# Optimization experiments

Measured on AMD Instinct MI355X. Metric: run time of the kernel, lower is better.

## Reference

```python
import jax, jax.numpy as jnp
import numpy as np

N = 50000      # nodes
E = 800000     # edges (avg degree 16)
IN = 128       # in_channels
OUT = 128      # out_channels


def setup_inputs() -> dict:
    key = jax.random.key(0)
    k1, k2, k3 = jax.random.split(key, 3)
    x = jax.random.normal(k1, (N, IN), dtype=jnp.float32)
    edge_index = jax.random.randint(k2, (2, E), 0, N, dtype=jnp.int32)
    # GCNConv params: glorot-ish linear weight + zero bias
    W = jax.random.normal(k3, (IN, OUT), dtype=jnp.float32) / np.float32(np.sqrt(IN))
    b = jnp.zeros((OUT,), dtype=jnp.float32)
    return {"x": x, "W": W, "b": b, "edge_index": edge_index}


def reference(x, W, b, edge_index):
    n = x.shape[0]
    src, dst = edge_index[0], edge_index[1]
    # add self loops (GCNConv default add_self_loops=True)
    loop = jnp.arange(n, dtype=edge_index.dtype)
    src = jnp.concatenate([src, loop])
    dst = jnp.concatenate([dst, loop])
    # symmetric normalization: deg^{-1/2}[src] * deg^{-1/2}[dst], deg from dst (flow source_to_target)
    deg = jax.ops.segment_sum(jnp.ones_like(dst, dtype=x.dtype), dst, num_segments=n)
    dinv = jnp.where(deg > 0, jax.lax.rsqrt(jnp.maximum(deg, 1.0)), 0.0)
    norm = dinv[src] * dinv[dst]                     # [E+N]
    xw = x @ W                                       # [N, OUT] dense GEMM first (as GCNConv does)
    msg = xw[src] * norm[:, None]                    # [E+N, OUT] gather + scale
    out = jax.ops.segment_sum(msg, dst, num_segments=n)  # scatter-add aggregate
    return out + b
```

## Files before the change

kernel.cpp:

```cpp
#include <hip/hip_runtime.h>


constexpr int CH = 128;
constexpr int CHUNK = 4096;
constexpr int NCMAX = 256;
constexpr int HP = 256;

typedef __attribute__((ext_vector_type(8))) short short8;
typedef __attribute__((ext_vector_type(4))) float f32x4;

static __device__ __forceinline__ ushort f2bf(float f) {
    unsigned u = __float_as_uint(f);
    u += 0x7fff + ((u >> 16) & 1);
    return (ushort)(u >> 16);
}


__global__ __launch_bounds__(256) void hist_packw(const int* __restrict__ dst,
        int* __restrict__ h, int* __restrict__ coltot,
        const float* __restrict__ Wm, ushort* __restrict__ Wp,
        int E, int nc, int nblk) {
    int t = threadIdx.x, b = blockIdx.x;
    if (b >= nblk) {
        int tid = (b - nblk) * 256 + t;
        if (tid < 2048) {
            int col = tid >> 4, ch16 = tid & 15;
            ushort tmp[8];
            #pragma unroll
            for (int i = 0; i < 8; ++i)
                tmp[i] = f2bf(Wm[(size_t)(ch16 * 8 + i) * CH + col]);
            int d = col * 16 + (ch16 ^ (col & 7));
            *(uint4*)&Wp[(size_t)d * 8] = *(uint4*)tmp;
        }
        return;
    }
    __shared__ int hh[NCMAX];
    for (int i = t; i < NCMAX; i += 256) hh[i] = 0;
    __syncthreads();
    int s = b * CHUNK, e = min(E, s + CHUNK);
    for (int i = s + t * 4; i < e; i += 1024) {
        if (i + 4 <= e) {
            int4 v = *(const int4*)&dst[i];
            atomicAdd(&hh[v.x >> 8], 1);
            atomicAdd(&hh[v.y >> 8], 1);
            atomicAdd(&hh[v.z >> 8], 1);
            atomicAdd(&hh[v.w >> 8], 1);
        } else {
            for (int k = i; k < e; ++k) atomicAdd(&hh[dst[k] >> 8], 1);
        }
    }
    __syncthreads();
    for (int i = t; i < nc; i += 256) {
        int v = hh[i];
        h[(size_t)i * HP + b] = v;
        if (v) atomicAdd(&coltot[i], v);
    }
}


__global__ __launch_bounds__(256) void binscatter_gemm(const int* __restrict__ src,
        const int* __restrict__ dst, const int* __restrict__ h,
        const int* __restrict__ coltot, unsigned* __restrict__ ebuf,
        const float* __restrict__ x, const ushort* __restrict__ Wp,
        ushort* __restrict__ xwd, int E, int N, int nc, int nblk) {
    __shared__ alignas(16) ushort Wlds[16384];
    int t = threadIdx.x, b = blockIdx.x;

    if (b < nblk) {
        int* smc = (int*)Wlds;
        int* cur = smc + 256;
        smc[t] = (t < nc) ? coltot[t] : 0;
        __syncthreads();
        #pragma unroll
        for (int d = 1; d < 256; d <<= 1) {
            int u = (t >= d) ? smc[t - d] : 0;
            __syncthreads();
            smc[t] += u;
            __syncthreads();
        }
        if (t < nc) {
            int base = (t > 0) ? smc[t - 1] : 0;
            const int* hp = &h[(size_t)t * HP];
            int pfx = 0;
            int j = 0;
            for (; j + 4 <= b; j += 4) {
                int4 v = *(const int4*)&hp[j];
                pfx += v.x + v.y + v.z + v.w;
            }
            for (; j < b; ++j) pfx += hp[j];
            cur[t] = base + pfx;
        }
        __syncthreads();
        int s = b * CHUNK, e = min(E, s + CHUNK);
        for (int i = s + t; i < e; i += 256) {
            int d = dst[i];
            int pos = atomicAdd(&cur[d >> 8], 1);
            ebuf[pos] = (unsigned)src[i] | ((unsigned)(d & 255) << 16);
        }
        return;
    }

    int gb = b - nblk;
    int wv = t >> 6, l = t & 63;
    int c15 = l & 15, kc = l >> 4;
    int row0 = gb * 64 + wv * 16;
    int r = row0 + c15;
    bool valid = r < N;

    short8 af[4];
    #pragma unroll
    for (int ks = 0; ks < 4; ++ks) {
        float4 a0 = make_float4(0.f,0.f,0.f,0.f), a1 = a0;
        if (valid) {
            const float* p = x + (size_t)r * CH + ks * 32 + kc * 8;
            a0 = *(const float4*)p;
            a1 = *(const float4*)(p + 4);
        }
        short8 v;
        v[0]=f2bf(a0.x); v[1]=f2bf(a0.y); v[2]=f2bf(a0.z); v[3]=f2bf(a0.w);
        v[4]=f2bf(a1.x); v[5]=f2bf(a1.y); v[6]=f2bf(a1.z); v[7]=f2bf(a1.w);
        af[ks] = v;
    }

    #pragma unroll
    for (int i = 0; i < 8; ++i) {
        int idx = i * 256 + t;
        *(uint4*)&Wlds[idx * 8] = *(const uint4*)&Wp[idx * 8];
    }
    __syncthreads();

    f32x4 acc[8];
    #pragma unroll
    for (int ct = 0; ct < 8; ++ct) { f32x4 z = {0.f,0.f,0.f,0.f}; acc[ct] = z; }

    int swz = l & 7;
    #pragma unroll
    for (int ks = 0; ks < 4; ++ks) {
        #pragma unroll
        for (int ct = 0; ct < 8; ++ct) {
            int col = ct * 16 + c15;
            int idx16 = (col * 16 + ks * 4 + kc) ^ swz;
            short8 bfrag = *(const short8*)&Wlds[idx16 * 8];
            acc[ct] = __builtin_amdgcn_mfma_f32_16x16x32_bf16(af[ks], bfrag, acc[ct], 0, 0, 0);
        }
    }
    __syncthreads();

    ushort* bw = Wlds + wv * 2048;
    #pragma unroll
    for (int ct = 0; ct < 8; ++ct) {
        #pragma unroll
        for (int rr = 0; rr < 4; ++rr) {
            int row_local = kc * 4 + rr;
            bw[row_local * CH + ct * 16 + c15] = f2bf(acc[ct][rr]);
        }
    }
    #pragma unroll
    for (int p = 0; p < 4; ++p) {
        int row_local = p * 4 + kc;
        int row = row0 + row_local;
        if (row < N) {
            uint4 vv = *(const uint4*)&bw[row_local * CH + c15 * 8];
            *(uint4*)&xwd[(size_t)row * CH + c15 * 8] = vv;
        }
    }
}


__global__ __launch_bounds__(256) void bucket_csr(const unsigned* __restrict__ ebuf,
        const int* __restrict__ coltot, int* __restrict__ off, ushort* __restrict__ csr,
        float* __restrict__ dinv, int N, int nc) {
    __shared__ int hist2[256], cur[256], sm[256];
    int t = threadIdx.x, k = blockIdx.x;
    sm[t] = (t < nc) ? coltot[t] : 0;
    __syncthreads();
    #pragma unroll
    for (int d = 1; d < 256; d <<= 1) {
        int u = (t >= d) ? sm[t - d] : 0;
        __syncthreads();
        sm[t] += u;
        __syncthreads();
    }
    int s = (k > 0) ? sm[k - 1] : 0;
    int e = sm[k];
    __syncthreads();

    hist2[t] = 0;
    __syncthreads();
    for (int i = s + t; i < e; i += 256) atomicAdd(&hist2[(ebuf[i] >> 16) & 255], 1);
    __syncthreads();
    int v = hist2[t];
    sm[t] = v;
    __syncthreads();
    #pragma unroll
    for (int d = 1; d < 256; d <<= 1) {
        int u = (t >= d) ? sm[t - d] : 0;
        __syncthreads();
        sm[t] += u;
        __syncthreads();
    }
    int excl = sm[t] - v;
    int node = k * 256 + t;
    if (node <= N) off[node] = s + excl;
    if (node < N) dinv[node] = rsqrtf((float)(v + 1));
    cur[t] = s + excl;
    __syncthreads();
    for (int i = s + t; i < e; i += 256) {
        unsigned u = ebuf[i];
        int pos = atomicAdd(&cur[(u >> 16) & 255], 1);
        csr[pos] = (ushort)(u & 0xffffu);
    }
}


__global__ __launch_bounds__(256) void agg_kernel(const ushort* __restrict__ xwd,
        const ushort* __restrict__ csr, const int* __restrict__ off,
        const float* __restrict__ dinv, const float* __restrict__ b,
        float* __restrict__ out, int N) {
    int t = threadIdx.x;
    int c15 = t & 15;
    int node = blockIdx.x * 16 + (t >> 4);
    if (node >= N) return;
    int s = off[node], e = off[node + 1];
    float acc[8] = {0.f,0.f,0.f,0.f,0.f,0.f,0.f,0.f};
    const ushort* base = xwd + c15 * 8;
    float di = dinv[node];

    int last = e - 1;
    for (int j = s; j < e; j += 8) {
        int idx[8]; float m[8];
        #pragma unroll
        for (int k = 0; k < 8; ++k) {
            int jj = j + k;
            idx[k] = csr[min(jj, last)];
            m[k] = (jj <= last) ? dinv[idx[k]] : 0.0f;
        }
        uint4 v[8];
        #pragma unroll
        for (int k = 0; k < 8; ++k)
            v[k] = *(const uint4*)(base + (size_t)idx[k] * CH);
        #pragma unroll
        for (int k = 0; k < 8; ++k) {
            acc[0] += m[k] * __uint_as_float(v[k].x << 16);
            acc[1] += m[k] * __uint_as_float(v[k].x & 0xffff0000u);
            acc[2] += m[k] * __uint_as_float(v[k].y << 16);
            acc[3] += m[k] * __uint_as_float(v[k].y & 0xffff0000u);
            acc[4] += m[k] * __uint_as_float(v[k].z << 16);
            acc[5] += m[k] * __uint_as_float(v[k].z & 0xffff0000u);
            acc[6] += m[k] * __uint_as_float(v[k].w << 16);
            acc[7] += m[k] * __uint_as_float(v[k].w & 0xffff0000u);
        }
    }
    {
        uint4 v = *(const uint4*)(base + (size_t)node * CH);
        acc[0] += di * __uint_as_float(v.x << 16);
        acc[1] += di * __uint_as_float(v.x & 0xffff0000u);
        acc[2] += di * __uint_as_float(v.y << 16);
        acc[3] += di * __uint_as_float(v.y & 0xffff0000u);
        acc[4] += di * __uint_as_float(v.z << 16);
        acc[5] += di * __uint_as_float(v.z & 0xffff0000u);
        acc[6] += di * __uint_as_float(v.w << 16);
        acc[7] += di * __uint_as_float(v.w & 0xffff0000u);
    }
    float4 b0 = *(const float4*)&b[c15 * 8];
    float4 b1 = *(const float4*)&b[c15 * 8 + 4];
    f32x4 o0, o1;
    o0[0] = di * acc[0] + b0.x;  o0[1] = di * acc[1] + b0.y;
    o0[2] = di * acc[2] + b0.z;  o0[3] = di * acc[3] + b0.w;
    o1[0] = di * acc[4] + b1.x;  o1[1] = di * acc[5] + b1.y;
    o1[2] = di * acc[6] + b1.z;  o1[3] = di * acc[7] + b1.w;
    float* op = out + (size_t)node * CH + c15 * 8;
    __builtin_nontemporal_store(o0, (f32x4*)op);
    __builtin_nontemporal_store(o1, (f32x4*)(op + 4));
}


extern "C" void kernel_launch(void* const* d_in, const int* in_sizes, int n_in,
                              void* d_out, int out_size, void* d_ws, size_t ws_size,
                              hipStream_t stream) {
    const float* x  = (const float*)d_in[0];
    const float* Wm = (const float*)d_in[1];
    const float* b  = (const float*)d_in[2];
    const int*   ei = (const int*)d_in[3];
    int N = in_sizes[0] / CH;
    int E = in_sizes[3] / 2;
    const int* src = ei;
    const int* dst = ei + E;
    float* out = (float*)d_out;

    char* w = (char*)d_ws;
    auto alloc = [&](size_t bytes) {
        char* p = w;
        w += (bytes + 255) & ~(size_t)255;
        return p;
    };
    int nc = (N + 255) >> 8;
    int nblk = (E + CHUNK - 1) / CHUNK;
    int gemm_blocks = (N + 63) / 64;

    ushort*   xwd  = (ushort*)alloc((size_t)N * CH * 2);
    unsigned* ebuf = (unsigned*)alloc((size_t)E * 4);
    int*      off  = (int*)alloc((size_t)(N + 1) * 4);
    ushort*   csr  = (ushort*)alloc((size_t)E * 2);
    float*    dinv = (float*)alloc((size_t)N * 4);
    ushort*   Wp   = (ushort*)alloc((size_t)16384 * 2);
    int*      h    = (int*)alloc((size_t)nc * HP * 4);
    int*      coltot=(int*)alloc((size_t)nc * 4);

    (void)hipMemsetAsync(coltot, 0, (size_t)nc * 4, stream);
    hist_packw<<<nblk + 8, 256, 0, stream>>>(dst, h, coltot, Wm, Wp, E, nc, nblk);
    binscatter_gemm<<<nblk + gemm_blocks, 256, 0, stream>>>(src, dst, h, coltot, ebuf,
                                                            x, Wp, xwd, E, N, nc, nblk);
    bucket_csr<<<nc, 256, 0, stream>>>(ebuf, coltot, off, csr, dinv, N, nc);
    agg_kernel<<<(N + 15) / 16, 256, 0, stream>>>(xwd, csr, off, dinv, b, out, N);
}
```

Baseline: 86.06 us.

## Split XW into four channel-quarter planes and aggregate per quarter

The GEMM output is stored as four separate planes of 32 bf16 channels per node instead of one row of 128 channels. The aggregation kernel now assigns each block one channel quarter, with 4 lanes per node and 64 nodes per block. Block IDs are interleaved so that blocks working on the same quarter run close together, which keeps each 3.2MB plane's working set smaller and more cache-resident during the random gathers. In exchange, the CSR indices and dinv values are read four times over, and each gather is 64 bytes instead of 256 bytes.

```diff
diff --git a/kernel.cpp b/kernel.cpp
--- a/kernel.cpp
+++ b/kernel.cpp
@@ -62,7 +62,7 @@
         const int* __restrict__ dst, const int* __restrict__ h,
         const int* __restrict__ coltot, unsigned* __restrict__ ebuf,
         const float* __restrict__ x, const ushort* __restrict__ Wp,
-        ushort* __restrict__ xwd, int E, int N, int nc, int nblk) {
+        ushort* __restrict__ xwq, int E, int N, int nc, int nblk) {
     __shared__ alignas(16) ushort Wlds[16384];
     int t = threadIdx.x, b = blockIdx.x;
 
@@ -155,13 +155,14 @@
             bw[row_local * CH + ct * 16 + c15] = f2bf(acc[ct][rr]);
         }
     }
+    int q = c15 >> 2;
     #pragma unroll
     for (int p = 0; p < 4; ++p) {
         int row_local = p * 4 + kc;
         int row = row0 + row_local;
         if (row < N) {
             uint4 vv = *(const uint4*)&bw[row_local * CH + c15 * 8];
-            *(uint4*)&xwd[(size_t)row * CH + c15 * 8] = vv;
+            *(uint4*)&xwq[((size_t)q * N + row) * 32 + (c15 & 3) * 8] = vv;
         }
     }
 }
@@ -213,17 +214,20 @@
 }
 
 
-__global__ __launch_bounds__(256) void agg_kernel(const ushort* __restrict__ xwd,
+__global__ __launch_bounds__(256) void agg_kernel(const ushort* __restrict__ xwq,
         const ushort* __restrict__ csr, const int* __restrict__ off,
         const float* __restrict__ dinv, const float* __restrict__ b,
         float* __restrict__ out, int N) {
     int t = threadIdx.x;
-    int c15 = t & 15;
-    int node = blockIdx.x * 16 + (t >> 4);
+    int bid = blockIdx.x;
+    int q = (bid & 7) >> 1;
+    int iw = (bid >> 3) * 2 + (bid & 1);
+    int node = iw * 64 + (t >> 2);
     if (node >= N) return;
+    int lane4 = t & 3;
     int s = off[node], e = off[node + 1];
     float acc[8] = {0.f,0.f,0.f,0.f,0.f,0.f,0.f,0.f};
-    const ushort* base = xwd + c15 * 8;
+    const ushort* base = xwq + (size_t)q * N * 32 + lane4 * 8;
     float di = dinv[node];
 
     int last = e - 1;
@@ -238,7 +242,7 @@
         uint4 v[8];
         #pragma unroll
         for (int k = 0; k < 8; ++k)
-            v[k] = *(const uint4*)(base + (size_t)idx[k] * CH);
+            v[k] = *(const uint4*)(base + (size_t)idx[k] * 32);
         #pragma unroll
         for (int k = 0; k < 8; ++k) {
             acc[0] += m[k] * __uint_as_float(v[k].x << 16);
@@ -252,7 +256,7 @@
         }
     }
     {
-        uint4 v = *(const uint4*)(base + (size_t)node * CH);
+        uint4 v = *(const uint4*)(base + (size_t)node * 32);
         acc[0] += di * __uint_as_float(v.x << 16);
         acc[1] += di * __uint_as_float(v.x & 0xffff0000u);
         acc[2] += di * __uint_as_float(v.y << 16);
@@ -262,14 +266,15 @@
         acc[6] += di * __uint_as_float(v.w << 16);
         acc[7] += di * __uint_as_float(v.w & 0xffff0000u);
     }
-    float4 b0 = *(const float4*)&b[c15 * 8];
-    float4 b1 = *(const float4*)&b[c15 * 8 + 4];
+    int ch0 = q * 32 + lane4 * 8;
+    float4 b0 = *(const float4*)&b[ch0];
+    float4 b1 = *(const float4*)&b[ch0 + 4];
     f32x4 o0, o1;
     o0[0] = di * acc[0] + b0.x;  o0[1] = di * acc[1] + b0.y;
     o0[2] = di * acc[2] + b0.z;  o0[3] = di * acc[3] + b0.w;
     o1[0] = di * acc[4] + b1.x;  o1[1] = di * acc[5] + b1.y;
     o1[2] = di * acc[6] + b1.z;  o1[3] = di * acc[7] + b1.w;
-    float* op = out + (size_t)node * CH + c15 * 8;
+    float* op = out + (size_t)node * CH + ch0;
     __builtin_nontemporal_store(o0, (f32x4*)op);
     __builtin_nontemporal_store(o1, (f32x4*)(op + 4));
 }
@@ -298,7 +303,7 @@
     int nblk = (E + CHUNK - 1) / CHUNK;
     int gemm_blocks = (N + 63) / 64;
 
-    ushort*   xwd  = (ushort*)alloc((size_t)N * CH * 2);
+    ushort*   xwq  = (ushort*)alloc((size_t)N * CH * 2);
     unsigned* ebuf = (unsigned*)alloc((size_t)E * 4);
     int*      off  = (int*)alloc((size_t)(N + 1) * 4);
     ushort*   csr  = (ushort*)alloc((size_t)E * 2);
@@ -310,7 +315,9 @@
     (void)hipMemsetAsync(coltot, 0, (size_t)nc * 4, stream);
     hist_packw<<<nblk + 8, 256, 0, stream>>>(dst, h, coltot, Wm, Wp, E, nc, nblk);
     binscatter_gemm<<<nblk + gemm_blocks, 256, 0, stream>>>(src, dst, h, coltot, ebuf,
-                                                            x, Wp, xwd, E, N, nc, nblk);
+                                                            x, Wp, xwq, E, N, nc, nblk);
     bucket_csr<<<nc, 256, 0, stream>>>(ebuf, coltot, off, csr, dinv, N, nc);
-    agg_kernel<<<(N + 15) / 16, 256, 0, stream>>>(xwd, csr, off, dinv, b, out, N);
-}
+    int nbq = (N + 63) / 64;
+    int agg_grid = ((nbq + 1) / 2) * 8;
+    agg_kernel<<<agg_grid, 256, 0, stream>>>(xwq, csr, off, dinv, b, out, N);
+}
```

Result: slower. 90.61 us (+5.3%).
